# Performance work log

Hardware: AMD Instinct MI355X
Metric: run time of the kernel (lower is better)

## Reference

```python
import jax, jax.numpy as jnp
import numpy as np

VOCAB = 1000000
EMBED_DIM = 64


def setup_inputs() -> dict:
    key = jax.random.key(0)
    embeddings = jax.random.normal(key, (VOCAB, EMBED_DIM), dtype=jnp.float32)
    return {"embeddings": embeddings, "user_id": 12345, "top_n": 10}


def reference(embeddings, user_id, top_n):
    # target_embedding = embedding_layer(user_id): [d]
    target = embeddings[user_id]  # [d]
    # cosine_similarity(target[None, :], all_embeddings): [V]
    dot = embeddings @ target  # [V]
    norm_t = jnp.linalg.norm(target)  # scalar (norm over axis=-1 of [1, d])
    norm_all = jnp.linalg.norm(embeddings, axis=-1)  # [V]
    sims = dot / (norm_t * norm_all)
    # tf.nn.top_k with k = top_n + 1, then drop the first (self) match
    top_vals, top_idx = jax.lax.top_k(sims, top_n + 1)
    return top_vals[1:], top_idx[1:]
```

## Files before the change

kernel.cpp:

```cpp
#include <hip/hip_runtime.h>
#include <cmath>
#include <climits>

#define EMBED 64
#define KTOP 11
#define NB   1024
#define BLOCK 256
#define NWAVE (BLOCK / 64)

__device__ __forceinline__ void topk_insert(float (&vals)[KTOP], int (&idxs)[KTOP],
                                            float v, int i) {
  float last = vals[KTOP - 1];
  if (v < last) return;
  if (v == last && i >= idxs[KTOP - 1]) return;
  float cv = v; int ci = i;
#pragma unroll
  for (int j = 0; j < KTOP; ++j) {
    bool better = (cv > vals[j]) || (cv == vals[j] && ci < idxs[j]);
    if (better) {
      float tv = vals[j]; int ti = idxs[j];
      vals[j] = cv; idxs[j] = ci;
      cv = tv; ci = ti;
    }
  }
}

__device__ __forceinline__ void wave_merge(float (&vals)[KTOP], int (&idxs)[KTOP],
                                           float* wv, int* wi, int lane) {
#pragma unroll
  for (int round = 0; round < KTOP; ++round) {
    float v = vals[0]; int i = idxs[0]; int l = lane;
#pragma unroll
    for (int off = 32; off > 0; off >>= 1) {
      float ov = __shfl_xor(v, off, 64);
      int   oi = __shfl_xor(i, off, 64);
      int   ol = __shfl_xor(l, off, 64);
      if (ov > v || (ov == v && oi < i)) { v = ov; i = oi; l = ol; }
    }
    if (l == lane) {
#pragma unroll
      for (int j = 0; j < KTOP - 1; ++j) { vals[j] = vals[j + 1]; idxs[j] = idxs[j + 1]; }
      vals[KTOP - 1] = -INFINITY; idxs[KTOP - 1] = INT_MAX;
    }
    if (lane == 0) { wv[round] = v; wi[round] = i; }
  }
}

__global__ __launch_bounds__(BLOCK) void sim_pass1(
    const float* __restrict__ emb, const int* __restrict__ user_id,
    float* __restrict__ cand_val, int* __restrict__ cand_idx, int V) {
  __shared__ float t[EMBED];
  __shared__ float wv[NWAVE * KTOP];
  __shared__ int   wi[NWAVE * KTOP];

  const int lane = threadIdx.x & 63;
  const int wid  = threadIdx.x >> 6;

  const int uid = *user_id;
  if (threadIdx.x < EMBED) t[threadIdx.x] = emb[(size_t)uid * EMBED + threadIdx.x];
  __syncthreads();

  float4 tv[EMBED / 4];
#pragma unroll
  for (int j = 0; j < EMBED / 4; ++j) tv[j] = ((const float4*)t)[j];

  float vals[KTOP]; int idxs[KTOP];
#pragma unroll
  for (int j = 0; j < KTOP; ++j) { vals[j] = -INFINITY; idxs[j] = INT_MAX; }

  const int stride = gridDim.x * BLOCK;
  for (int r = blockIdx.x * BLOCK + threadIdx.x; r < V; r += stride) {
    const float4* rp = (const float4*)(emb + (size_t)r * EMBED);
    float dot = 0.f, nr = 0.f;
#pragma unroll
    for (int j = 0; j < EMBED / 4; ++j) {
      float4 v = rp[j];
      dot = fmaf(v.x, tv[j].x, dot); dot = fmaf(v.y, tv[j].y, dot);
      dot = fmaf(v.z, tv[j].z, dot); dot = fmaf(v.w, tv[j].w, dot);
      nr  = fmaf(v.x, v.x, nr);      nr  = fmaf(v.y, v.y, nr);
      nr  = fmaf(v.z, v.z, nr);      nr  = fmaf(v.w, v.w, nr);
    }
    float sim = dot / sqrtf(nr);
    topk_insert(vals, idxs, sim, r);
  }

  wave_merge(vals, idxs, &wv[wid * KTOP], &wi[wid * KTOP], lane);
  __syncthreads();

  if (wid == 0) {
    float v = (lane < NWAVE * KTOP) ? wv[lane] : -INFINITY;
    int   i = (lane < NWAVE * KTOP) ? wi[lane] : INT_MAX;
#pragma unroll
    for (int round = 0; round < KTOP; ++round) {
      float bv = v; int bi = i; int bl = lane;
#pragma unroll
      for (int off = 32; off > 0; off >>= 1) {
        float ov = __shfl_xor(bv, off, 64);
        int   oi = __shfl_xor(bi, off, 64);
        int   ol = __shfl_xor(bl, off, 64);
        if (ov > bv || (ov == bv && oi < bi)) { bv = ov; bi = oi; bl = ol; }
      }
      if (bl == lane) { v = -INFINITY; i = INT_MAX; }
      if (lane == 0) {
        cand_val[blockIdx.x * KTOP + round] = bv;
        cand_idx[blockIdx.x * KTOP + round] = bi;
      }
    }
  }
}

__global__ __launch_bounds__(BLOCK) void sim_pass2(
    const float* __restrict__ emb, const int* __restrict__ user_id,
    const float* __restrict__ cand_val, const int* __restrict__ cand_idx,
    float* __restrict__ out, int topn, int ncand) {
  __shared__ float wv[NWAVE * KTOP];
  __shared__ int   wi[NWAVE * KTOP];
  __shared__ float s_nt;

  const int lane = threadIdx.x & 63;
  const int wid  = threadIdx.x >> 6;

  if (wid == 0) {
    const int uid = *user_id;
    float x = (lane < EMBED) ? emb[(size_t)uid * EMBED + lane] : 0.f;
    float s = x * x;
#pragma unroll
    for (int off = 32; off > 0; off >>= 1) s += __shfl_xor(s, off, 64);
    if (lane == 0) s_nt = sqrtf(s);
  }

  float vals[KTOP]; int idxs[KTOP];
#pragma unroll
  for (int j = 0; j < KTOP; ++j) { vals[j] = -INFINITY; idxs[j] = INT_MAX; }

  for (int c = threadIdx.x; c < ncand; c += BLOCK)
    topk_insert(vals, idxs, cand_val[c], cand_idx[c]);

  wave_merge(vals, idxs, &wv[wid * KTOP], &wi[wid * KTOP], lane);
  __syncthreads();

  if (wid == 0) {
    float v = (lane < NWAVE * KTOP) ? wv[lane] : -INFINITY;
    int   i = (lane < NWAVE * KTOP) ? wi[lane] : INT_MAX;
    const float nt = s_nt;
#pragma unroll
    for (int round = 0; round < KTOP; ++round) {
      float bv = v; int bi = i; int bl = lane;
#pragma unroll
      for (int off = 32; off > 0; off >>= 1) {
        float ov = __shfl_xor(bv, off, 64);
        int   oi = __shfl_xor(bi, off, 64);
        int   ol = __shfl_xor(bl, off, 64);
        if (ov > bv || (ov == bv && oi < bi)) { bv = ov; bi = oi; bl = ol; }
      }
      if (bl == lane) { v = -INFINITY; i = INT_MAX; }
      if (lane == 0 && round >= 1 && round <= topn) {
        out[round - 1]        = bv / nt;
        out[topn + round - 1] = (float)bi;
      }
    }
  }
}

extern "C" void kernel_launch(void* const* d_in, const int* in_sizes, int n_in,
                              void* d_out, int out_size, void* d_ws, size_t ws_size,
                              hipStream_t stream) {
  const float* emb = (const float*)d_in[0];
  const int*   uid = (const int*)d_in[1];
  const int V    = in_sizes[0] / EMBED;
  const int topn = out_size / 2;

  float* cand_val = (float*)d_ws;
  int*   cand_idx = (int*)((char*)d_ws + (size_t)NB * KTOP * sizeof(float));

  sim_pass1<<<NB, BLOCK, 0, stream>>>(emb, uid, cand_val, cand_idx, V);
  sim_pass2<<<1, BLOCK, 0, stream>>>(emb, uid, cand_val, cand_idx,
                                     (float*)d_out, topn, NB * KTOP);
}
```

Before: 453.3 us.

## Coalesce embedding reads by assigning 16 lanes per row with shuffle reduction

Replaces the one-thread-per-row scan with a wave-per-tile scheme. Each group of 16 lanes reads one 64-float row as float4s, so a wave's loads are contiguous. Partial dot products and norms are combined with xor shuffles, and one designated lane per row inserts the similarity into its top-k list. The aim is to remove the strided, uncoalesced per-thread row loads, at the cost of extra shuffle instructions and a more serialized top-k insert.

```diff
diff --git a/kernel.cpp b/kernel.cpp
--- a/kernel.cpp
+++ b/kernel.cpp
@@ -60,28 +60,40 @@
   if (threadIdx.x < EMBED) t[threadIdx.x] = emb[(size_t)uid * EMBED + threadIdx.x];
   __syncthreads();
 
-  float4 tv[EMBED / 4];
-#pragma unroll
-  for (int j = 0; j < EMBED / 4; ++j) tv[j] = ((const float4*)t)[j];
+  const float4 tgt = ((const float4*)t)[lane & 15];
 
   float vals[KTOP]; int idxs[KTOP];
 #pragma unroll
   for (int j = 0; j < KTOP; ++j) { vals[j] = -INFINITY; idxs[j] = INT_MAX; }
 
-  const int stride = gridDim.x * BLOCK;
-  for (int r = blockIdx.x * BLOCK + threadIdx.x; r < V; r += stride) {
-    const float4* rp = (const float4*)(emb + (size_t)r * EMBED);
-    float dot = 0.f, nr = 0.f;
+  const int gw = blockIdx.x * NWAVE + wid;
+  const int nW = NB * NWAVE;
+  const int nTiles = (V + 63) >> 6;
+
+  for (int tile = gw; tile < nTiles; tile += nW) {
+    const int rowBase = tile << 6;
+    const float4* p = (const float4*)(emb + (size_t)rowBase * EMBED);
 #pragma unroll
-    for (int j = 0; j < EMBED / 4; ++j) {
-      float4 v = rp[j];
-      dot = fmaf(v.x, tv[j].x, dot); dot = fmaf(v.y, tv[j].y, dot);
-      dot = fmaf(v.z, tv[j].z, dot); dot = fmaf(v.w, tv[j].w, dot);
-      nr  = fmaf(v.x, v.x, nr);      nr  = fmaf(v.y, v.y, nr);
-      nr  = fmaf(v.z, v.z, nr);      nr  = fmaf(v.w, v.w, nr);
+    for (int t16 = 0; t16 < 16; ++t16) {
+      const int row = rowBase + t16 * 4 + (lane >> 4);
+      float dot = 0.f, nr = 0.f;
+      if (row < V) {
+        float4 v = p[t16 * 64 + lane];
+        dot = fmaf(v.x, tgt.x, dot); dot = fmaf(v.y, tgt.y, dot);
+        dot = fmaf(v.z, tgt.z, dot); dot = fmaf(v.w, tgt.w, dot);
+        nr  = fmaf(v.x, v.x, nr);    nr  = fmaf(v.y, v.y, nr);
+        nr  = fmaf(v.z, v.z, nr);    nr  = fmaf(v.w, v.w, nr);
+      }
+#pragma unroll
+      for (int off = 1; off < 16; off <<= 1) {
+        dot += __shfl_xor(dot, off, 64);
+        nr  += __shfl_xor(nr,  off, 64);
+      }
+      if ((lane & 15) == t16 && row < V) {
+        float sim = dot / sqrtf(nr);
+        topk_insert(vals, idxs, sim, row);
+      }
     }
-    float sim = dot / sqrtf(nr);
-    topk_insert(vals, idxs, sim, r);
   }
 
   wave_merge(vals, idxs, &wv[wid * KTOP], &wi[wid * KTOP], lane);
```

New measurement: 481.4 us. +6.2%, slower.

## Stream embedding tiles into LDS via async global_load_lds double buffering

Applied to the files above, without the earlier changes.

In the first pass, each wave now copies 64-row tiles of the embedding table into its own double-buffered LDS region using global_load_lds, which turns the strided per-thread row reads into fully coalesced 16-byte loads. While the next tile is in flight, the wave computes dot products and norms from LDS, with a lane-rotated column order to avoid bank conflicts. Grid and block sizes change to 512 blocks of 128 threads to fit 64KB of LDS per block. The cost is manual vmcnt waits and a heavy LDS footprint that limits occupancy, plus clamped addressing for the tail tile.

```diff
diff --git a/kernel.cpp b/kernel.cpp
--- a/kernel.cpp
+++ b/kernel.cpp
@@ -4,9 +4,15 @@
 
 #define EMBED 64
 #define KTOP 11
-#define NB   1024
-#define BLOCK 256
-#define NWAVE (BLOCK / 64)
+#define NB   512
+#define BLOCK1 128
+#define NW1  (BLOCK1 / 64)
+#define BLOCK2 256
+#define NW2  (BLOCK2 / 64)
+#define TILE_BYTES 16384
+
+typedef const __attribute__((address_space(1))) void gv_t;
+typedef __attribute__((address_space(3))) void lv_t;
 
 __device__ __forceinline__ void topk_insert(float (&vals)[KTOP], int (&idxs)[KTOP],
                                             float v, int i) {
@@ -46,50 +52,102 @@
   }
 }
 
-__global__ __launch_bounds__(BLOCK) void sim_pass1(
+__device__ __forceinline__ void dma_tile(const char* g, size_t byteBase,
+                                         int lane, char* lds) {
+#pragma unroll
+  for (int j = 0; j < 16; ++j) {
+    __builtin_amdgcn_global_load_lds(
+        (gv_t*)(g + byteBase + (size_t)j * 1024 + (size_t)lane * 16),
+        (lv_t*)(lds + j * 1024), 16, 0, 0);
+  }
+}
+
+__device__ __forceinline__ void dma_tile_clamped(const char* g, size_t byteBase,
+                                                 int lane, char* lds, size_t maxOff) {
+#pragma unroll
+  for (int j = 0; j < 16; ++j) {
+    size_t off = byteBase + (size_t)j * 1024 + (size_t)lane * 16;
+    if (off > maxOff) off = maxOff;
+    __builtin_amdgcn_global_load_lds(
+        (gv_t*)(g + off), (lv_t*)(lds + j * 1024), 16, 0, 0);
+  }
+}
+
+__global__ __launch_bounds__(BLOCK1) void sim_pass1(
     const float* __restrict__ emb, const int* __restrict__ user_id,
     float* __restrict__ cand_val, int* __restrict__ cand_idx, int V) {
-  __shared__ float t[EMBED];
-  __shared__ float wv[NWAVE * KTOP];
-  __shared__ int   wi[NWAVE * KTOP];
+  __shared__ __align__(16) char smem[2 * NW1 * TILE_BYTES];
 
   const int lane = threadIdx.x & 63;
   const int wid  = threadIdx.x >> 6;
-
-  const int uid = *user_id;
-  if (threadIdx.x < EMBED) t[threadIdx.x] = emb[(size_t)uid * EMBED + threadIdx.x];
+  const int uid  = *user_id;
+
+  const float4* trow = (const float4*)(emb + (size_t)uid * EMBED);
+  float4 tv[16];
+#pragma unroll
+  for (int j = 0; j < 16; ++j) tv[j] = trow[(j + lane) & 15];
+
+  float vals[KTOP]; int idxs[KTOP];
+#pragma unroll
+  for (int j = 0; j < KTOP; ++j) { vals[j] = -INFINITY; idxs[j] = INT_MAX; }
+
+  const int gw = blockIdx.x * NW1 + wid;
+  const int nW = NB * NW1;
+  const int nTiles = (V + 63) >> 6;
+  const char* g = (const char*)emb;
+  const size_t maxOff = (size_t)V * 256 - 16;
+  char* myLds = smem + wid * (2 * TILE_BYTES);
+
+  int p = 0;
+  int tile = gw;
+  if (tile < nTiles) {
+    if (((size_t)tile * 64 + 64) * 256 - 16 <= maxOff + 0)
+      dma_tile(g, (size_t)tile << 14, lane, myLds);
+    else
+      dma_tile_clamped(g, (size_t)tile << 14, lane, myLds, maxOff);
+  }
+
+  for (; tile < nTiles; tile += nW) {
+    const int next = tile + nW;
+    const bool pf = next < nTiles;
+    if (pf) {
+      char* nb = myLds + ((p ^ 1) * TILE_BYTES);
+      if ((size_t)(next + 1) * 64 * 256 - 16 <= maxOff)
+        dma_tile(g, (size_t)next << 14, lane, nb);
+      else
+        dma_tile_clamped(g, (size_t)next << 14, lane, nb, maxOff);
+      asm volatile("s_waitcnt vmcnt(16)" ::: "memory");
+    } else {
+      asm volatile("s_waitcnt vmcnt(0)" ::: "memory");
+    }
+
+    const char* lb = myLds + p * TILE_BYTES + lane * 256;
+    float dot = 0.f, nr = 0.f;
+#pragma unroll
+    for (int j = 0; j < 16; ++j) {
+      const int c = (j + lane) & 15;
+      float4 v = *(const float4*)(lb + c * 16);
+      float4 t = tv[j];
+      dot = fmaf(v.x, t.x, dot); dot = fmaf(v.y, t.y, dot);
+      dot = fmaf(v.z, t.z, dot); dot = fmaf(v.w, t.w, dot);
+      nr  = fmaf(v.x, v.x, nr);  nr  = fmaf(v.y, v.y, nr);
+      nr  = fmaf(v.z, v.z, nr);  nr  = fmaf(v.w, v.w, nr);
+    }
+    const int row = (tile << 6) + lane;
+    if (row < V)
+      topk_insert(vals, idxs, dot / sqrtf(nr), row);
+    p ^= 1;
+  }
+
   __syncthreads();
-
-  float4 tv[EMBED / 4];
-#pragma unroll
-  for (int j = 0; j < EMBED / 4; ++j) tv[j] = ((const float4*)t)[j];
-
-  float vals[KTOP]; int idxs[KTOP];
-#pragma unroll
-  for (int j = 0; j < KTOP; ++j) { vals[j] = -INFINITY; idxs[j] = INT_MAX; }
-
-  const int stride = gridDim.x * BLOCK;
-  for (int r = blockIdx.x * BLOCK + threadIdx.x; r < V; r += stride) {
-    const float4* rp = (const float4*)(emb + (size_t)r * EMBED);
-    float dot = 0.f, nr = 0.f;
-#pragma unroll
-    for (int j = 0; j < EMBED / 4; ++j) {
-      float4 v = rp[j];
-      dot = fmaf(v.x, tv[j].x, dot); dot = fmaf(v.y, tv[j].y, dot);
-      dot = fmaf(v.z, tv[j].z, dot); dot = fmaf(v.w, tv[j].w, dot);
-      nr  = fmaf(v.x, v.x, nr);      nr  = fmaf(v.y, v.y, nr);
-      nr  = fmaf(v.z, v.z, nr);      nr  = fmaf(v.w, v.w, nr);
-    }
-    float sim = dot / sqrtf(nr);
-    topk_insert(vals, idxs, sim, r);
-  }
-
+  float* wv = (float*)smem;
+  int*   wi = (int*)(smem + NW1 * KTOP * sizeof(float));
   wave_merge(vals, idxs, &wv[wid * KTOP], &wi[wid * KTOP], lane);
   __syncthreads();
 
   if (wid == 0) {
-    float v = (lane < NWAVE * KTOP) ? wv[lane] : -INFINITY;
-    int   i = (lane < NWAVE * KTOP) ? wi[lane] : INT_MAX;
+    float v = (lane < NW1 * KTOP) ? wv[lane] : -INFINITY;
+    int   i = (lane < NW1 * KTOP) ? wi[lane] : INT_MAX;
 #pragma unroll
     for (int round = 0; round < KTOP; ++round) {
       float bv = v; int bi = i; int bl = lane;
@@ -109,12 +167,12 @@
   }
 }
 
-__global__ __launch_bounds__(BLOCK) void sim_pass2(
+__global__ __launch_bounds__(BLOCK2) void sim_pass2(
     const float* __restrict__ emb, const int* __restrict__ user_id,
     const float* __restrict__ cand_val, const int* __restrict__ cand_idx,
     float* __restrict__ out, int topn, int ncand) {
-  __shared__ float wv[NWAVE * KTOP];
-  __shared__ int   wi[NWAVE * KTOP];
+  __shared__ float wv[NW2 * KTOP];
+  __shared__ int   wi[NW2 * KTOP];
   __shared__ float s_nt;
 
   const int lane = threadIdx.x & 63;
@@ -133,15 +191,15 @@
 #pragma unroll
   for (int j = 0; j < KTOP; ++j) { vals[j] = -INFINITY; idxs[j] = INT_MAX; }
 
-  for (int c = threadIdx.x; c < ncand; c += BLOCK)
+  for (int c = threadIdx.x; c < ncand; c += BLOCK2)
     topk_insert(vals, idxs, cand_val[c], cand_idx[c]);
 
   wave_merge(vals, idxs, &wv[wid * KTOP], &wi[wid * KTOP], lane);
   __syncthreads();
 
   if (wid == 0) {
-    float v = (lane < NWAVE * KTOP) ? wv[lane] : -INFINITY;
-    int   i = (lane < NWAVE * KTOP) ? wi[lane] : INT_MAX;
+    float v = (lane < NW2 * KTOP) ? wv[lane] : -INFINITY;
+    int   i = (lane < NW2 * KTOP) ? wi[lane] : INT_MAX;
     const float nt = s_nt;
 #pragma unroll
     for (int round = 0; round < KTOP; ++round) {
@@ -173,7 +231,7 @@
   float* cand_val = (float*)d_ws;
   int*   cand_idx = (int*)((char*)d_ws + (size_t)NB * KTOP * sizeof(float));
 
-  sim_pass1<<<NB, BLOCK, 0, stream>>>(emb, uid, cand_val, cand_idx, V);
-  sim_pass2<<<1, BLOCK, 0, stream>>>(emb, uid, cand_val, cand_idx,
-                                     (float*)d_out, topn, NB * KTOP);
-}
+  sim_pass1<<<NB, BLOCK1, 0, stream>>>(emb, uid, cand_val, cand_idx, V);
+  sim_pass2<<<1, BLOCK2, 0, stream>>>(emb, uid, cand_val, cand_idx,
+                                      (float*)d_out, topn, NB * KTOP);
+}
```

Result: faster. 407.3 us (-10.2%).

## Coalesce embedding reads with wave-per-64-row tiles and shuffle transpose-reduce

Applied to the files above, without the earlier changes.

Pass 1 now assigns a 64-row tile to each wavefront. Lanes load consecutive float4s, so every global load is fully coalesced, where before each thread strode through its own 256-byte row. The partial dot products and norms are reduced across 16 lanes with a butterfly shuffle transpose, leaving one row's result per lane. The grid is halved to 512 blocks with a launch-bounds occupancy hint, and the target vector is loaded straight from global memory rather than through LDS. The cost is extra shuffle instructions and higher register pressure from holding 16 float4s per lane.

```diff
diff --git a/kernel.cpp b/kernel.cpp
--- a/kernel.cpp
+++ b/kernel.cpp
@@ -4,9 +4,11 @@
 
 #define EMBED 64
 #define KTOP 11
-#define NB   1024
-#define BLOCK 256
-#define NWAVE (BLOCK / 64)
+#define NB   512
+#define BLOCK1 256
+#define NW1  (BLOCK1 / 64)
+#define BLOCK2 256
+#define NW2  (BLOCK2 / 64)
 
 __device__ __forceinline__ void topk_insert(float (&vals)[KTOP], int (&idxs)[KTOP],
                                             float v, int i) {
@@ -46,50 +48,75 @@
   }
 }
 
-__global__ __launch_bounds__(BLOCK) void sim_pass1(
+__global__ __launch_bounds__(BLOCK1, 2) void sim_pass1(
     const float* __restrict__ emb, const int* __restrict__ user_id,
     float* __restrict__ cand_val, int* __restrict__ cand_idx, int V) {
-  __shared__ float t[EMBED];
-  __shared__ float wv[NWAVE * KTOP];
-  __shared__ int   wi[NWAVE * KTOP];
+  __shared__ float wv[NW1 * KTOP];
+  __shared__ int   wi[NW1 * KTOP];
 
   const int lane = threadIdx.x & 63;
   const int wid  = threadIdx.x >> 6;
-
-  const int uid = *user_id;
-  if (threadIdx.x < EMBED) t[threadIdx.x] = emb[(size_t)uid * EMBED + threadIdx.x];
-  __syncthreads();
-
-  float4 tv[EMBED / 4];
-#pragma unroll
-  for (int j = 0; j < EMBED / 4; ++j) tv[j] = ((const float4*)t)[j];
+  const int uid  = *user_id;
+
+  const float4 tgt = ((const float4*)(emb + (size_t)uid * EMBED))[lane & 15];
 
   float vals[KTOP]; int idxs[KTOP];
 #pragma unroll
   for (int j = 0; j < KTOP; ++j) { vals[j] = -INFINITY; idxs[j] = INT_MAX; }
 
-  const int stride = gridDim.x * BLOCK;
-  for (int r = blockIdx.x * BLOCK + threadIdx.x; r < V; r += stride) {
-    const float4* rp = (const float4*)(emb + (size_t)r * EMBED);
-    float dot = 0.f, nr = 0.f;
-#pragma unroll
-    for (int j = 0; j < EMBED / 4; ++j) {
-      float4 v = rp[j];
-      dot = fmaf(v.x, tv[j].x, dot); dot = fmaf(v.y, tv[j].y, dot);
-      dot = fmaf(v.z, tv[j].z, dot); dot = fmaf(v.w, tv[j].w, dot);
-      nr  = fmaf(v.x, v.x, nr);      nr  = fmaf(v.y, v.y, nr);
-      nr  = fmaf(v.z, v.z, nr);      nr  = fmaf(v.w, v.w, nr);
-    }
-    float sim = dot / sqrtf(nr);
-    topk_insert(vals, idxs, sim, r);
+  const int gw = blockIdx.x * NW1 + wid;
+  const int nW = NB * NW1;
+  const int nTiles = (V + 63) >> 6;
+  const float4* base = (const float4*)emb;
+  const size_t maxQ = (size_t)V * 16 - 1;
+
+  for (int tile = gw; tile < nTiles; tile += nW) {
+    const size_t q0 = (size_t)tile * 1024 + lane;
+    float4 v[16];
+#pragma unroll
+    for (int j = 0; j < 16; ++j) {
+      size_t q = q0 + (size_t)j * 64;
+      if (q > maxQ) q = maxQ;
+      v[j] = base[q];
+    }
+
+    float d[16], n[16];
+#pragma unroll
+    for (int j = 0; j < 16; ++j) {
+      float4 x = v[j];
+      float dd =        x.x * tgt.x;
+      dd = fmaf(x.y, tgt.y, dd); dd = fmaf(x.z, tgt.z, dd); dd = fmaf(x.w, tgt.w, dd);
+      float nn =        x.x * x.x;
+      nn = fmaf(x.y, x.y, nn);   nn = fmaf(x.z, x.z, nn);   nn = fmaf(x.w, x.w, nn);
+      d[j] = dd; n[j] = nn;
+    }
+
+#pragma unroll
+    for (int st = 0; st < 4; ++st) {
+      const int m = 1 << st;
+      const int b = (lane >> st) & 1;
+#pragma unroll
+      for (int k = 0; k < (16 >> (st + 1)); ++k) {
+        float dk = b ? d[2 * k + 1] : d[2 * k];
+        float ds = b ? d[2 * k]     : d[2 * k + 1];
+        float nk = b ? n[2 * k + 1] : n[2 * k];
+        float ns = b ? n[2 * k]     : n[2 * k + 1];
+        d[k] = dk + __shfl_xor(ds, m, 64);
+        n[k] = nk + __shfl_xor(ns, m, 64);
+      }
+    }
+
+    const int r = (tile << 6) + ((lane & 15) << 2) + (lane >> 4);
+    if (r < V)
+      topk_insert(vals, idxs, d[0] / sqrtf(n[0]), r);
   }
 
   wave_merge(vals, idxs, &wv[wid * KTOP], &wi[wid * KTOP], lane);
   __syncthreads();
 
   if (wid == 0) {
-    float v = (lane < NWAVE * KTOP) ? wv[lane] : -INFINITY;
-    int   i = (lane < NWAVE * KTOP) ? wi[lane] : INT_MAX;
+    float v = (lane < NW1 * KTOP) ? wv[lane] : -INFINITY;
+    int   i = (lane < NW1 * KTOP) ? wi[lane] : INT_MAX;
 #pragma unroll
     for (int round = 0; round < KTOP; ++round) {
       float bv = v; int bi = i; int bl = lane;
@@ -109,12 +136,12 @@
   }
 }
 
-__global__ __launch_bounds__(BLOCK) void sim_pass2(
+__global__ __launch_bounds__(BLOCK2) void sim_pass2(
     const float* __restrict__ emb, const int* __restrict__ user_id,
     const float* __restrict__ cand_val, const int* __restrict__ cand_idx,
     float* __restrict__ out, int topn, int ncand) {
-  __shared__ float wv[NWAVE * KTOP];
-  __shared__ int   wi[NWAVE * KTOP];
+  __shared__ float wv[NW2 * KTOP];
+  __shared__ int   wi[NW2 * KTOP];
   __shared__ float s_nt;
 
   const int lane = threadIdx.x & 63;
@@ -133,15 +160,15 @@
 #pragma unroll
   for (int j = 0; j < KTOP; ++j) { vals[j] = -INFINITY; idxs[j] = INT_MAX; }
 
-  for (int c = threadIdx.x; c < ncand; c += BLOCK)
+  for (int c = threadIdx.x; c < ncand; c += BLOCK2)
     topk_insert(vals, idxs, cand_val[c], cand_idx[c]);
 
   wave_merge(vals, idxs, &wv[wid * KTOP], &wi[wid * KTOP], lane);
   __syncthreads();
 
   if (wid == 0) {
-    float v = (lane < NWAVE * KTOP) ? wv[lane] : -INFINITY;
-    int   i = (lane < NWAVE * KTOP) ? wi[lane] : INT_MAX;
+    float v = (lane < NW2 * KTOP) ? wv[lane] : -INFINITY;
+    int   i = (lane < NW2 * KTOP) ? wi[lane] : INT_MAX;
     const float nt = s_nt;
 #pragma unroll
     for (int round = 0; round < KTOP; ++round) {
@@ -173,7 +200,7 @@
   float* cand_val = (float*)d_ws;
   int*   cand_idx = (int*)((char*)d_ws + (size_t)NB * KTOP * sizeof(float));
 
-  sim_pass1<<<NB, BLOCK, 0, stream>>>(emb, uid, cand_val, cand_idx, V);
-  sim_pass2<<<1, BLOCK, 0, stream>>>(emb, uid, cand_val, cand_idx,
-                                     (float*)d_out, topn, NB * KTOP);
-}
+  sim_pass1<<<NB, BLOCK1, 0, stream>>>(emb, uid, cand_val, cand_idx, V);
+  sim_pass2<<<1, BLOCK2, 0, stream>>>(emb, uid, cand_val, cand_idx,
+                                      (float*)d_out, topn, NB * KTOP);
+}
```

Result: faster. 405.7 us (-10.5%).
